# Performance work log

Measured on AMD Instinct MI355X. Metric: run time of the kernel, lower is better.

## Reference

```python
import jax, jax.numpy as jnp
import numpy as np

B, S, D, H, DK = 2, 2048, 2048, 16, 128
ALIBI_SLOPE = 8.0
NEG = -1e9  # finite stand-in for -inf so gradients stay finite


def setup_inputs() -> dict:
    key = jax.random.key(0)
    ks = jax.random.split(key, 8)
    states = jax.random.normal(ks[0], (B, S, D), jnp.float32)
    # causal ALiBi-style additive bias: -(i-j) for j<=i else very negative
    pos = jnp.arange(S)
    dist = pos[None, :] - pos[:, None]  # j - i
    bias = jnp.where(dist <= 0, dist.astype(jnp.float32), NEG)
    bias_mask = jnp.broadcast_to(bias[None], (B, S, S))
    # per-head scale: exp2(-((h+1)*slope/H))
    head_scale = jnp.exp2(-((jnp.arange(H) + 1.0) * ALIBI_SLOPE / H)).astype(jnp.float32)
    init = lambda k, shp: jax.random.normal(k, shp, jnp.float32) * (shp[-1] ** -0.5)
    return {
        'states': states,
        'bias_mask': bias_mask,
        'head_scale': head_scale,
        'Wq': init(ks[1], (D, D)), 'bq': jnp.zeros((D,), jnp.float32),
        'Wk': init(ks[2], (D, D)), 'bk': jnp.zeros((D,), jnp.float32),
        'Wv': init(ks[3], (D, D)), 'bv': jnp.zeros((D,), jnp.float32),
        'Wg': init(ks[4], (H, D)), 'bg': jnp.zeros((H,), jnp.float32),
        'Wo': init(ks[5], (D, D)), 'bo': jnp.zeros((D,), jnp.float32),
    }


def reference(states, bias_mask, head_scale, Wq, bq, Wk, bk, Wv, bv, Wg, bg, Wo, bo):
    b, s, d = states.shape
    key_scale = DK ** -0.5
    proj = lambda x, W, bias: x @ W.T + bias
    # [b,s,d] -> [b,h,s,dk]
    q = proj(states, Wq, bq).reshape(b, s, H, DK).transpose(0, 2, 1, 3)
    k = proj(states, Wk, bk).reshape(b, s, H, DK).transpose(0, 2, 1, 3)
    v = proj(states, Wv, bv).reshape(b, s, H, DK).transpose(0, 2, 1, 3)
    # additive per-head ALiBi bias: [b,1,s,s] * [1,h,1,1]
    bias = bias_mask[:, None, :, :] * head_scale[None, :, None, None]
    scores = jnp.einsum('bhqd,bhkd->bhqk', q, k) * key_scale + bias
    attn = jax.nn.softmax(scores, axis=-1)
    o = jnp.einsum('bhqk,bhkd->bhqd', attn, v).transpose(0, 2, 1, 3)  # [b,s,h,dk]
    g = jax.nn.sigmoid(proj(states, Wg, bg))  # [b,s,h]
    o = o * g[..., None]
    return proj(o.reshape(b, s, d), Wo, bo)
```

## Files before the change

kernel.cpp:

```cpp
#include <hip/hip_runtime.h>

#define SEQ  2048
#define NROW 4096
#define KDIM 2048
#define NH   16
#define DKH  128
#define CSUB 20.0f
#define LOG2E 1.44269504088896f

typedef unsigned int u32;
typedef unsigned short u16;
typedef __attribute__((ext_vector_type(8))) __bf16 bf16x8;
typedef __attribute__((ext_vector_type(4))) float f32x4;
typedef __attribute__((ext_vector_type(4))) u16 u16x4;

struct alignas(16) U4 { u32 x, y, z, w; };

__device__ __forceinline__ u16 f2bf(float f) {
  u32 u = __builtin_bit_cast(u32, f);
  u32 r = (u + 0x7fffu + ((u >> 16) & 1u)) >> 16;
  return (u16)r;
}
__device__ __forceinline__ u16 f2bf_n(float f) {
  __bf16 h = (__bf16)f;
  return __builtin_bit_cast(u16, h);
}
__device__ __forceinline__ bf16x8 asb(U4 v) { return __builtin_bit_cast(bf16x8, v); }
__device__ __forceinline__ float exp2a(float x) {
  float r;
  asm("v_exp_f32 %0, %1" : "=v"(r) : "v"(x));
  return r;
}

__device__ __forceinline__ void gl2lds16(const u16* g, u16* l) {
  __builtin_amdgcn_global_load_lds(
      (const __attribute__((address_space(1))) void*)g,
      (__attribute__((address_space(3))) void*)l, 16, 0, 0);
}

__global__ __launch_bounds__(256)
void cvtk(const float* __restrict__ src, u16* __restrict__ dst, int n)
{
  const int i = (blockIdx.x * 256 + threadIdx.x) * 4;
  if (i < n) {
    f32x4 v = *(const f32x4*)(src + i);
    u16x4 o;
#pragma unroll
    for (int j = 0; j < 4; ++j) o[j] = f2bf(v[j]);
    *(u16x4*)(dst + i) = o;
  }
}

__global__ __launch_bounds__(256, 2)
void qkvg(const u16* __restrict__ A, const u16* __restrict__ B,
          const float* __restrict__ bq, const float* __restrict__ bk,
          const float* __restrict__ bv, u16* __restrict__ Qw,
          u16* __restrict__ Kw, u16* __restrict__ Vw)
{
  __shared__ alignas(16) u16 As[128 * 32];
  __shared__ alignas(16) u16 Bs[128 * 32];
  const int tid = threadIdx.x;
  const int lane = tid & 63, wave = tid >> 6;
  const int wm = wave >> 1, wn = wave & 1;
  const int l15 = lane & 15, quad = lane >> 4;
  const int m0 = blockIdx.y * 128, n0 = blockIdx.x * 128;

  f32x4 acc[4][4];
#pragma unroll
  for (int i = 0; i < 4; ++i)
#pragma unroll
    for (int j = 0; j < 4; ++j) acc[i][j] = {0.f, 0.f, 0.f, 0.f};

  const int gr = lane >> 2;
  const int gc = (lane & 3) * 8;

  for (int kk = 0; kk < KDIM; kk += 32) {
#pragma unroll
    for (int it = 0; it < 2; ++it) {
      const int r0 = wave * 32 + it * 16;
      gl2lds16(A + (size_t)(m0 + r0 + gr) * KDIM + kk + gc, As + r0 * 32);
      gl2lds16(B + (size_t)(n0 + r0 + gr) * KDIM + kk + gc, Bs + r0 * 32);
    }
    __syncthreads();
    U4 af[4], bg[4];
#pragma unroll
    for (int t = 0; t < 4; ++t) {
      af[t] = *(const U4*)(As + (wm * 64 + t * 16 + l15) * 32 + quad * 8);
      bg[t] = *(const U4*)(Bs + (wn * 64 + t * 16 + l15) * 32 + quad * 8);
    }
#pragma unroll
    for (int mt = 0; mt < 4; ++mt)
#pragma unroll
      for (int nt = 0; nt < 4; ++nt)
        acc[mt][nt] = __builtin_amdgcn_mfma_f32_16x16x32_bf16(
            asb(af[mt]), asb(bg[nt]), acc[mt][nt], 0, 0, 0);
    __syncthreads();
  }

  const int seg = n0 >> 11;
  const float* bp = seg == 0 ? bq : (seg == 1 ? bk : bv);
  u16* Cq = seg == 0 ? Qw : Kw;

#pragma unroll
  for (int mt = 0; mt < 4; ++mt) {
    const int rowb = m0 + wm * 64 + mt * 16 + quad * 4;
    const int b = rowb >> 11, srow = rowb & (SEQ - 1);
#pragma unroll
    for (int nt = 0; nt < 4; ++nt) {
      const int col6 = n0 + wn * 64 + nt * 16 + l15;
      const int col = col6 & 2047;
      const int h = col >> 7, dk = col & 127;
      const float bvl = bp[col];
      if (seg == 2) {
        u16x4 pk;
#pragma unroll
        for (int r = 0; r < 4; ++r) pk[r] = f2bf(acc[mt][nt][r] + bvl);
        const size_t idx = ((size_t)(b * NH + h) * DKH + dk) * SEQ + srow;
        *(u16x4*)(Vw + idx) = pk;
      } else {
#pragma unroll
        for (int r = 0; r < 4; ++r) {
          const size_t idx = ((size_t)(b * NH + h) * SEQ + (srow + r)) * DKH + dk;
          Cq[idx] = f2bf(acc[mt][nt][r] + bvl);
        }
      }
    }
  }
}

__global__ __launch_bounds__(256, 2)
void gemm_bt(const u16* __restrict__ A, const u16* __restrict__ B,
             const float* __restrict__ bias, float* __restrict__ Cf)
{
  __shared__ alignas(16) u16 As[128 * 32];
  __shared__ alignas(16) u16 Bs[128 * 32];
  const int tid = threadIdx.x;
  const int lane = tid & 63, wave = tid >> 6;
  const int wm = wave >> 1, wn = wave & 1;
  const int l15 = lane & 15, quad = lane >> 4;
  const int m0 = blockIdx.y * 128, n0 = blockIdx.x * 128;

  f32x4 acc[4][4];
#pragma unroll
  for (int i = 0; i < 4; ++i)
#pragma unroll
    for (int j = 0; j < 4; ++j) acc[i][j] = {0.f, 0.f, 0.f, 0.f};

  const int gr = lane >> 2;
  const int gc = (lane & 3) * 8;

  for (int kk = 0; kk < KDIM; kk += 32) {
#pragma unroll
    for (int it = 0; it < 2; ++it) {
      const int r0 = wave * 32 + it * 16;
      gl2lds16(A + (size_t)(m0 + r0 + gr) * KDIM + kk + gc, As + r0 * 32);
      gl2lds16(B + (size_t)(n0 + r0 + gr) * KDIM + kk + gc, Bs + r0 * 32);
    }
    __syncthreads();
    U4 af[4], bg[4];
#pragma unroll
    for (int t = 0; t < 4; ++t) {
      af[t] = *(const U4*)(As + (wm * 64 + t * 16 + l15) * 32 + quad * 8);
      bg[t] = *(const U4*)(Bs + (wn * 64 + t * 16 + l15) * 32 + quad * 8);
    }
#pragma unroll
    for (int mt = 0; mt < 4; ++mt)
#pragma unroll
      for (int nt = 0; nt < 4; ++nt)
        acc[mt][nt] = __builtin_amdgcn_mfma_f32_16x16x32_bf16(
            asb(af[mt]), asb(bg[nt]), acc[mt][nt], 0, 0, 0);
    __syncthreads();
  }

#pragma unroll
  for (int mt = 0; mt < 4; ++mt) {
    const int rowb = m0 + wm * 64 + mt * 16 + quad * 4;
#pragma unroll
    for (int nt = 0; nt < 4; ++nt) {
      const int col = n0 + wn * 64 + nt * 16 + l15;
      const float bv = bias[col];
#pragma unroll
      for (int r = 0; r < 4; ++r)
        Cf[(size_t)(rowb + r) * KDIM + col] = acc[mt][nt][r] + bv;
    }
  }
}

__global__ __launch_bounds__(256)
void gateg(const u16* __restrict__ X, const float* __restrict__ Wg,
           const float* __restrict__ bg, float* __restrict__ G)
{
  __shared__ float red[4][16][16];
  const int tid = threadIdx.x;
  const int lane = tid & 63, wave = tid >> 6;
  const int l15 = lane & 15, quad = lane >> 4;
  const int m0 = blockIdx.x * 16;

  const u16*  Xp = X + (size_t)(m0 + l15) * KDIM + wave * 512 + quad * 8;
  const float* Wp = Wg + (size_t)l15 * KDIM + wave * 512 + quad * 8;

  f32x4 acc = {0.f, 0.f, 0.f, 0.f};
#pragma unroll
  for (int kk = 0; kk < 512; kk += 32) {
    U4 a = *(const U4*)(Xp + kk);
    f32x4 w0 = *(const f32x4*)(Wp + kk);
    f32x4 w1 = *(const f32x4*)(Wp + kk + 4);
    U4 bw;
    bw.x = (u32)f2bf(w0[0]) | ((u32)f2bf(w0[1]) << 16);
    bw.y = (u32)f2bf(w0[2]) | ((u32)f2bf(w0[3]) << 16);
    bw.z = (u32)f2bf(w1[0]) | ((u32)f2bf(w1[1]) << 16);
    bw.w = (u32)f2bf(w1[2]) | ((u32)f2bf(w1[3]) << 16);
    acc = __builtin_amdgcn_mfma_f32_16x16x32_bf16(asb(a), asb(bw), acc, 0, 0, 0);
  }
#pragma unroll
  for (int r = 0; r < 4; ++r) red[wave][quad * 4 + r][l15] = acc[r];
  __syncthreads();
  const int row = tid >> 4, head = tid & 15;
  float s = bg[head];
#pragma unroll
  for (int w = 0; w < 4; ++w) s += red[w][row][head];
  G[(size_t)(m0 + row) * NH + head] = 1.f / (1.f + __expf(-s));
}

__device__ __forceinline__ void stage_kv(const u16* __restrict__ Kh,
                                         const u16* __restrict__ Vh,
                                         int kk, u16* Ksb, u16* Vsb,
                                         int wave, int lane)
{
  const int rK = lane >> 4, cK = lane & 15;
  const int rV = lane >> 3, cV = lane & 7;
#pragma unroll
  for (int j = 0; j < 4; ++j) {
    const int r0k = wave * 16 + j * 4;
    const int xk = ((j & 1) << 2) | rK;
    gl2lds16(Kh + (size_t)(kk + r0k + rK) * DKH + ((cK ^ xk) * 8),
             Ksb + r0k * 128);
    const int r0v = wave * 32 + j * 8;
    gl2lds16(Vh + (size_t)(r0v + rV) * SEQ + kk + ((cV ^ rV) * 8),
             Vsb + r0v * 64);
  }
}

__global__ __launch_bounds__(256, 2)
void attnk(const u16* __restrict__ Q, const u16* __restrict__ Km,
           const u16* __restrict__ Vt, const float* __restrict__ hsc,
           const float* __restrict__ G, u16* __restrict__ O)
{
  __shared__ alignas(16) u16 Ks[2][64 * 128];
  __shared__ alignas(16) u16 Vs[2][128 * 64];
  __shared__ alignas(16) u16 Ps[4][16 * 72];
  const int tid = threadIdx.x;
  const int lane = tid & 63, wave = tid >> 6;
  const int l15 = lane & 15, quad = lane >> 4;
  const int l7x = l15 & 7;
  const int qt = 31 - blockIdx.y, bh = blockIdx.x;
  const int b = bh >> 4, h = bh & 15;
  const size_t hoff = (size_t)bh * SEQ * DKH;
  const u16* Qh = Q + hoff;
  const u16* Kh = Km + hoff;
  const u16* Vh = Vt + hoff;
  const float hs2 = hsc[h] * LOG2E;
  const float ks2 = 0.08838834764831845f * LOG2E;
  const float csub2 = CSUB * LOG2E;
  const float dstep = 64.0f * hs2;

  const int q0 = qt * 64 + wave * 16;
  const int ntile = qt + 1;

  U4 aq[4];
#pragma unroll
  for (int c = 0; c < 4; ++c)
    aq[c] = *(const U4*)(Qh + (size_t)(q0 + l15) * DKH + c * 32 + quad * 8);

  float base[4][4];
#pragma unroll
  for (int r = 0; r < 4; ++r) {
    const int i = q0 + quad * 4 + r;
#pragma unroll
    for (int nt = 0; nt < 4; ++nt)
      base[r][nt] = (float)(nt * 16 + l15 - i) * hs2 - csub2;
  }

  f32x4 oacc[8];
#pragma unroll
  for (int c = 0; c < 8; ++c) oacc[c] = {0.f, 0.f, 0.f, 0.f};
  float l_lane[4] = {0.f, 0.f, 0.f, 0.f};

  stage_kv(Kh, Vh, 0, Ks[0], Vs[0], wave, lane);

  for (int t = 0; t < ntile; ++t) {
    const int kk = t * 64;
    const int cb = t & 1;
    __syncthreads();
    if (t + 1 < ntile)
      stage_kv(Kh, Vh, kk + 64, Ks[cb ^ 1], Vs[cb ^ 1], wave, lane);

    f32x4 sf[4];
#pragma unroll
    for (int nt = 0; nt < 4; ++nt) {
      f32x4 s = {0.f, 0.f, 0.f, 0.f};
#pragma unroll
      for (int c = 0; c < 4; ++c) {
        U4 bk = *(const U4*)(Ks[cb] + (nt * 16 + l15) * 128 +
                             (((c * 4 + quad) ^ l7x) * 8));
        s = __builtin_amdgcn_mfma_f32_16x16x32_bf16(asb(aq[c]), asb(bk), s, 0, 0, 0);
      }
      sf[nt] = s;
    }

    u16* Pw = &Ps[wave][0];
    const float tf = (float)t;
    if (t + 1 < ntile) {
#pragma unroll
      for (int r = 0; r < 4; ++r) {
#pragma unroll
        for (int nt = 0; nt < 4; ++nt) {
          const float p = exp2a(fmaf(sf[nt][r], ks2, fmaf(tf, dstep, base[r][nt])));
          l_lane[r] += p;
          Pw[(quad * 4 + r) * 72 + nt * 16 + l15] = f2bf_n(p);
        }
      }
    } else {
#pragma unroll
      for (int r = 0; r < 4; ++r) {
        const int i = q0 + quad * 4 + r;
#pragma unroll
        for (int nt = 0; nt < 4; ++nt) {
          const int j = kk + nt * 16 + l15;
          float p = 0.f;
          if (j <= i)
            p = exp2a(fmaf(sf[nt][r], ks2, fmaf(tf, dstep, base[r][nt])));
          l_lane[r] += p;
          Pw[(quad * 4 + r) * 72 + nt * 16 + l15] = f2bf_n(p);
        }
      }
    }
    asm volatile("s_waitcnt lgkmcnt(0)" ::: "memory");
    __builtin_amdgcn_sched_barrier(0);
    U4 pf0 = *(const U4*)(Pw + l15 * 72 + quad * 8);
    U4 pf1 = *(const U4*)(Pw + l15 * 72 + 32 + quad * 8);
#pragma unroll
    for (int c = 0; c < 8; ++c) {
      U4 bv0 = *(const U4*)(Vs[cb] + (c * 16 + l15) * 64 + ((quad ^ l7x) * 8));
      U4 bv1 = *(const U4*)(Vs[cb] + (c * 16 + l15) * 64 + (((quad + 4) ^ l7x) * 8));
      oacc[c] = __builtin_amdgcn_mfma_f32_16x16x32_bf16(asb(pf0), asb(bv0), oacc[c], 0, 0, 0);
      oacc[c] = __builtin_amdgcn_mfma_f32_16x16x32_bf16(asb(pf1), asb(bv1), oacc[c], 0, 0, 0);
    }
  }

  float sc[4];
#pragma unroll
  for (int r = 0; r < 4; ++r) {
#pragma unroll
    for (int d = 1; d < 16; d <<= 1)
      l_lane[r] += __shfl_xor(l_lane[r], d, 64);
    const int i = q0 + quad * 4 + r;
    sc[r] = G[(size_t)(b * SEQ + i) * NH + h] / l_lane[r];
  }

  __syncthreads();
  u16* OL = &Ks[0][0] + wave * 2112;
#pragma unroll
  for (int c = 0; c < 8; ++c)
#pragma unroll
    for (int r = 0; r < 4; ++r)
      OL[(quad * 4 + r) * 132 + c * 16 + l15] = f2bf_n(oacc[c][r] * sc[r]);
  __syncthreads();
#pragma unroll
  for (int o = 0; o < 4; ++o) {
    const int row = o * 4 + quad;
    U4 val = *(const U4*)(OL + row * 132 + l15 * 8);
    *(U4*)(O + ((size_t)(b * SEQ + q0 + row) * NH + h) * DKH + l15 * 8) = val;
  }
}

extern "C" void kernel_launch(void* const* d_in, const int* in_sizes, int n_in,
                              void* d_out, int out_size, void* d_ws, size_t ws_size,
                              hipStream_t stream)
{
  const float* states = (const float*)d_in[0];
  const float* hscale = (const float*)d_in[2];
  const float* Wq = (const float*)d_in[3];
  const float* bq = (const float*)d_in[4];
  const float* Wk = (const float*)d_in[5];
  const float* bk = (const float*)d_in[6];
  const float* Wv = (const float*)d_in[7];
  const float* bv = (const float*)d_in[8];
  const float* Wg = (const float*)d_in[9];
  const float* bg = (const float*)d_in[10];
  const float* Wo = (const float*)d_in[11];
  const float* bo = (const float*)d_in[12];
  float* out = (float*)d_out;

  char* ws = (char*)d_ws;
  const size_t MB = 1024 * 1024;
  u16* S16  = (u16*)(ws);
  u16* Qw   = (u16*)(ws + 16 * MB);
  u16* Kw   = (u16*)(ws + 32 * MB);
  u16* Vw   = (u16*)(ws + 48 * MB);
  u16* W16  = (u16*)(ws + 64 * MB);
  u16* Ow   = (u16*)(ws + 64 * MB);
  u16* Wo16 = (u16*)(ws + 80 * MB);
  float* Gw = out;

  const int NW = KDIM * KDIM;
  const int NS = NROW * KDIM;
  dim3 blk(256);

  cvtk<<<dim3(NS / 1024), blk, 0, stream>>>(states, S16, NS);
  gateg<<<dim3(NROW / 16), blk, 0, stream>>>(S16, Wg, bg, Gw);
  cvtk<<<dim3(NW / 1024), blk, 0, stream>>>(Wq, W16, NW);
  cvtk<<<dim3(NW / 1024), blk, 0, stream>>>(Wk, W16 + NW, NW);
  cvtk<<<dim3(NW / 1024), blk, 0, stream>>>(Wv, W16 + 2 * (size_t)NW, NW);
  qkvg<<<dim3(48, 32), blk, 0, stream>>>(S16, W16, bq, bk, bv, Qw, Kw, Vw);
  attnk<<<dim3(32, 32), blk, 0, stream>>>(Qw, Kw, Vw, hscale, Gw, Ow);
  cvtk<<<dim3(NW / 1024), blk, 0, stream>>>(Wo, Wo16, NW);
  gemm_bt<<<dim3(16, 32), blk, 0, stream>>>(Ow, Wo16, bo, out);
}
```

Before: 420.9 us.

## Double-buffer LDS in projection GEMMs, merge weight conversions, use native bf16 cast

Both projection GEMMs now use two LDS buffers, so the next K-slice is fetched with global_load_lds while MFMAs run on the current one, and one barrier per iteration is dropped. The three Wq/Wk/Wv conversion launches become a single launch with a 3-row grid. Manual rounding to bf16 is replaced by the native __bf16 cast. The cost is twice the LDS per block, which may limit occupancy, plus a possible difference in rounding behaviour.

```diff
diff --git a/kernel.cpp b/kernel.cpp
--- a/kernel.cpp
+++ b/kernel.cpp
@@ -46,8 +46,38 @@
     f32x4 v = *(const f32x4*)(src + i);
     u16x4 o;
 #pragma unroll
-    for (int j = 0; j < 4; ++j) o[j] = f2bf(v[j]);
+    for (int j = 0; j < 4; ++j) o[j] = f2bf_n(v[j]);
     *(u16x4*)(dst + i) = o;
+  }
+}
+
+__global__ __launch_bounds__(256)
+void cvt3k(const float* __restrict__ s0, const float* __restrict__ s1,
+           const float* __restrict__ s2, u16* __restrict__ dst, int n)
+{
+  const float* s = blockIdx.y == 0 ? s0 : (blockIdx.y == 1 ? s1 : s2);
+  u16* d = dst + (size_t)blockIdx.y * n;
+  const int i = (blockIdx.x * 256 + threadIdx.x) * 4;
+  if (i < n) {
+    f32x4 v = *(const f32x4*)(s + i);
+    u16x4 o;
+#pragma unroll
+    for (int j = 0; j < 4; ++j) o[j] = f2bf_n(v[j]);
+    *(u16x4*)(d + i) = o;
+  }
+}
+
+__device__ __forceinline__ void stage_ab(const u16* __restrict__ A,
+                                         const u16* __restrict__ B,
+                                         int m0, int n0, int kk,
+                                         u16* Asb, u16* Bsb,
+                                         int wave, int gr, int gc)
+{
+#pragma unroll
+  for (int it = 0; it < 2; ++it) {
+    const int r0 = wave * 32 + it * 16;
+    gl2lds16(A + (size_t)(m0 + r0 + gr) * KDIM + kk + gc, Asb + r0 * 32);
+    gl2lds16(B + (size_t)(n0 + r0 + gr) * KDIM + kk + gc, Bsb + r0 * 32);
   }
 }
 
@@ -57,8 +87,8 @@
           const float* __restrict__ bv, u16* __restrict__ Qw,
           u16* __restrict__ Kw, u16* __restrict__ Vw)
 {
-  __shared__ alignas(16) u16 As[128 * 32];
-  __shared__ alignas(16) u16 Bs[128 * 32];
+  __shared__ alignas(16) u16 As[2][128 * 32];
+  __shared__ alignas(16) u16 Bs[2][128 * 32];
   const int tid = threadIdx.x;
   const int lane = tid & 63, wave = tid >> 6;
   const int wm = wave >> 1, wn = wave & 1;
@@ -74,19 +104,19 @@
   const int gr = lane >> 2;
   const int gc = (lane & 3) * 8;
 
-  for (int kk = 0; kk < KDIM; kk += 32) {
-#pragma unroll
-    for (int it = 0; it < 2; ++it) {
-      const int r0 = wave * 32 + it * 16;
-      gl2lds16(A + (size_t)(m0 + r0 + gr) * KDIM + kk + gc, As + r0 * 32);
-      gl2lds16(B + (size_t)(n0 + r0 + gr) * KDIM + kk + gc, Bs + r0 * 32);
-    }
+  stage_ab(A, B, m0, n0, 0, As[0], Bs[0], wave, gr, gc);
+
+  const int NKI = KDIM / 32;
+  for (int ki = 0; ki < NKI; ++ki) {
+    const int cb = ki & 1;
     __syncthreads();
+    if (ki + 1 < NKI)
+      stage_ab(A, B, m0, n0, (ki + 1) * 32, As[cb ^ 1], Bs[cb ^ 1], wave, gr, gc);
     U4 af[4], bg[4];
 #pragma unroll
     for (int t = 0; t < 4; ++t) {
-      af[t] = *(const U4*)(As + (wm * 64 + t * 16 + l15) * 32 + quad * 8);
-      bg[t] = *(const U4*)(Bs + (wn * 64 + t * 16 + l15) * 32 + quad * 8);
+      af[t] = *(const U4*)(As[cb] + (wm * 64 + t * 16 + l15) * 32 + quad * 8);
+      bg[t] = *(const U4*)(Bs[cb] + (wn * 64 + t * 16 + l15) * 32 + quad * 8);
     }
 #pragma unroll
     for (int mt = 0; mt < 4; ++mt)
@@ -94,7 +124,6 @@
       for (int nt = 0; nt < 4; ++nt)
         acc[mt][nt] = __builtin_amdgcn_mfma_f32_16x16x32_bf16(
             asb(af[mt]), asb(bg[nt]), acc[mt][nt], 0, 0, 0);
-    __syncthreads();
   }
 
   const int seg = n0 >> 11;
@@ -114,14 +143,14 @@
       if (seg == 2) {
         u16x4 pk;
 #pragma unroll
-        for (int r = 0; r < 4; ++r) pk[r] = f2bf(acc[mt][nt][r] + bvl);
+        for (int r = 0; r < 4; ++r) pk[r] = f2bf_n(acc[mt][nt][r] + bvl);
         const size_t idx = ((size_t)(b * NH + h) * DKH + dk) * SEQ + srow;
         *(u16x4*)(Vw + idx) = pk;
       } else {
 #pragma unroll
         for (int r = 0; r < 4; ++r) {
           const size_t idx = ((size_t)(b * NH + h) * SEQ + (srow + r)) * DKH + dk;
-          Cq[idx] = f2bf(acc[mt][nt][r] + bvl);
+          Cq[idx] = f2bf_n(acc[mt][nt][r] + bvl);
         }
       }
     }
@@ -132,8 +161,8 @@
 void gemm_bt(const u16* __restrict__ A, const u16* __restrict__ B,
              const float* __restrict__ bias, float* __restrict__ Cf)
 {
-  __shared__ alignas(16) u16 As[128 * 32];
-  __shared__ alignas(16) u16 Bs[128 * 32];
+  __shared__ alignas(16) u16 As[2][128 * 32];
+  __shared__ alignas(16) u16 Bs[2][128 * 32];
   const int tid = threadIdx.x;
   const int lane = tid & 63, wave = tid >> 6;
   const int wm = wave >> 1, wn = wave & 1;
@@ -149,19 +178,19 @@
   const int gr = lane >> 2;
   const int gc = (lane & 3) * 8;
 
-  for (int kk = 0; kk < KDIM; kk += 32) {
-#pragma unroll
-    for (int it = 0; it < 2; ++it) {
-      const int r0 = wave * 32 + it * 16;
-      gl2lds16(A + (size_t)(m0 + r0 + gr) * KDIM + kk + gc, As + r0 * 32);
-      gl2lds16(B + (size_t)(n0 + r0 + gr) * KDIM + kk + gc, Bs + r0 * 32);
-    }
+  stage_ab(A, B, m0, n0, 0, As[0], Bs[0], wave, gr, gc);
+
+  const int NKI = KDIM / 32;
+  for (int ki = 0; ki < NKI; ++ki) {
+    const int cb = ki & 1;
     __syncthreads();
+    if (ki + 1 < NKI)
+      stage_ab(A, B, m0, n0, (ki + 1) * 32, As[cb ^ 1], Bs[cb ^ 1], wave, gr, gc);
     U4 af[4], bg[4];
 #pragma unroll
     for (int t = 0; t < 4; ++t) {
-      af[t] = *(const U4*)(As + (wm * 64 + t * 16 + l15) * 32 + quad * 8);
-      bg[t] = *(const U4*)(Bs + (wn * 64 + t * 16 + l15) * 32 + quad * 8);
+      af[t] = *(const U4*)(As[cb] + (wm * 64 + t * 16 + l15) * 32 + quad * 8);
+      bg[t] = *(const U4*)(Bs[cb] + (wn * 64 + t * 16 + l15) * 32 + quad * 8);
     }
 #pragma unroll
     for (int mt = 0; mt < 4; ++mt)
@@ -169,7 +198,6 @@
       for (int nt = 0; nt < 4; ++nt)
         acc[mt][nt] = __builtin_amdgcn_mfma_f32_16x16x32_bf16(
             asb(af[mt]), asb(bg[nt]), acc[mt][nt], 0, 0, 0);
-    __syncthreads();
   }
 
 #pragma unroll
@@ -206,10 +234,10 @@
     f32x4 w0 = *(const f32x4*)(Wp + kk);
     f32x4 w1 = *(const f32x4*)(Wp + kk + 4);
     U4 bw;
-    bw.x = (u32)f2bf(w0[0]) | ((u32)f2bf(w0[1]) << 16);
-    bw.y = (u32)f2bf(w0[2]) | ((u32)f2bf(w0[3]) << 16);
-    bw.z = (u32)f2bf(w1[0]) | ((u32)f2bf(w1[1]) << 16);
-    bw.w = (u32)f2bf(w1[2]) | ((u32)f2bf(w1[3]) << 16);
+    bw.x = (u32)f2bf_n(w0[0]) | ((u32)f2bf_n(w0[1]) << 16);
+    bw.y = (u32)f2bf_n(w0[2]) | ((u32)f2bf_n(w0[3]) << 16);
+    bw.z = (u32)f2bf_n(w1[0]) | ((u32)f2bf_n(w1[1]) << 16);
+    bw.w = (u32)f2bf_n(w1[2]) | ((u32)f2bf_n(w1[3]) << 16);
     acc = __builtin_amdgcn_mfma_f32_16x16x32_bf16(asb(a), asb(bw), acc, 0, 0, 0);
   }
 #pragma unroll
@@ -409,9 +437,7 @@
 
   cvtk<<<dim3(NS / 1024), blk, 0, stream>>>(states, S16, NS);
   gateg<<<dim3(NROW / 16), blk, 0, stream>>>(S16, Wg, bg, Gw);
-  cvtk<<<dim3(NW / 1024), blk, 0, stream>>>(Wq, W16, NW);
-  cvtk<<<dim3(NW / 1024), blk, 0, stream>>>(Wk, W16 + NW, NW);
-  cvtk<<<dim3(NW / 1024), blk, 0, stream>>>(Wv, W16 + 2 * (size_t)NW, NW);
+  cvt3k<<<dim3(NW / 1024, 3), blk, 0, stream>>>(Wq, Wk, Wv, W16, NW);
   qkvg<<<dim3(48, 32), blk, 0, stream>>>(S16, W16, bq, bk, bv, Qw, Kw, Vw);
   attnk<<<dim3(32, 32), blk, 0, stream>>>(Qw, Kw, Vw, hscale, Gw, Ow);
   cvtk<<<dim3(NW / 1024), blk, 0, stream>>>(Wo, Wo16, NW);
```

Result: no change. 427.6 us (+1.6%).
